# Kernel optimization log

Hardware: AMD Instinct MI355X
Metric: run time of the kernel (lower is better)

The kernel has to match this reference:

```python
import jax, jax.numpy as jnp
import numpy as np

B, L, E, H = 8, 1024, 512, 8
E2 = 2 * E
EPS = 1e-5


def _spectral_fc(x, w, fw, fb, n):
    # rfft along feature dim, multiply by rfft of learned filter w (1,n), irfft back, then Linear
    xf = jnp.fft.rfft(x, axis=2, norm='ortho')          # [B,L,n//2+1] complex
    wf = jnp.fft.rfft(w, axis=1, norm='ortho')          # [1,n//2+1] complex
    y = jnp.fft.irfft(xf * wf, n=n, axis=2, norm='ortho')
    return y @ fw + fb


def _layernorm(x, g, b):
    m = jnp.mean(x, axis=-1, keepdims=True)
    v = jnp.mean(jnp.square(x - m), axis=-1, keepdims=True)
    return (x - m) * jax.lax.rsqrt(v + EPS) * g + b


def setup_inputs() -> dict:
    key = jax.random.key(0)
    ks = jax.random.split(key, 32)
    s = 0.02

    def lin_w(k, i, o):
        return (jax.random.normal(k, (i, o), jnp.float32) / np.sqrt(i)).astype(jnp.float32)

    def layer_params(k0, k1, n):
        return (s * jax.random.normal(k0, (1, n), jnp.float32), lin_w(k1, n, n), jnp.zeros((n,), jnp.float32))

    attn_w, attn_fw, attn_fb = layer_params(ks[1], ks[2], E)
    ln0_w, ln0_fw, ln0_fb = layer_params(ks[3], ks[4], E)
    ln1_w, ln1_fw, ln1_fb = layer_params(ks[5], ks[6], E)
    ln2_w, ln2_fw, ln2_fb = layer_params(ks[7], ks[8], E)
    ln3_w, ln3_fw, ln3_fb = layer_params(ks[9], ks[10], E2)
    ln4_w, ln4_fw, ln4_fb = layer_params(ks[11], ks[12], E2)

    return {
        'x': jax.random.normal(ks[0], (B, L, E), jnp.float32),
        'attn_w': attn_w, 'attn_fw': attn_fw, 'attn_fb': attn_fb,
        'ln0_w': ln0_w, 'ln0_fw': ln0_fw, 'ln0_fb': ln0_fb,
        'ln1_w': ln1_w, 'ln1_fw': ln1_fw, 'ln1_fb': ln1_fb,
        'ln2_w': ln2_w, 'ln2_fw': ln2_fw, 'ln2_fb': ln2_fb,
        'ln3_w': ln3_w, 'ln3_fw': ln3_fw, 'ln3_fb': ln3_fb,
        'ln4_w': ln4_w, 'ln4_fw': ln4_fw, 'ln4_fb': ln4_fb,
        'n1_g': jnp.ones((E,), jnp.float32), 'n1_b': jnp.zeros((E,), jnp.float32),
        'n2_g': jnp.ones((E,), jnp.float32), 'n2_b': jnp.zeros((E,), jnp.float32),
    }


def reference(x, attn_w, attn_fw, attn_fb,
              ln0_w, ln0_fw, ln0_fb, ln1_w, ln1_fw, ln1_fb,
              ln2_w, ln2_fw, ln2_fb, ln3_w, ln3_fw, ln3_fb,
              ln4_w, ln4_fw, ln4_fb, n1_g, n1_b, n2_g, n2_b):
    q = _spectral_fc(x, attn_w, attn_fw, attn_fb, E).reshape(B, L, H, E // H)
    scores = jnp.einsum('blhe,bshe->bhls', q, q) * (1.0 / np.sqrt(E))
    A = jax.nn.softmax(scores, axis=-1)
    new_x = jnp.einsum('bhls,bshd->blhd', A, q).reshape(B, L, E)

    x1 = _layernorm(x + new_x, n1_g, n1_b)
    x_ln = jax.nn.gelu(_spectral_fc(x1, ln0_w, ln0_fw, ln0_fb, E), approximate=False)
    x2 = x1 - x_ln
    h = jax.nn.sigmoid(_spectral_fc(x2, ln1_w, ln1_fw, ln1_fb, E)) * _spectral_fc(x2, ln2_w, ln2_fw, ln2_fb, E)
    out = jnp.concatenate((new_x, x_ln), axis=-1)  # [B,L,2E]
    out = jax.nn.sigmoid(_spectral_fc(out, ln3_w, ln3_fw, ln3_fb, E2)) * _spectral_fc(out, ln4_w, ln4_fw, ln4_fb, E2)
    return (_layernorm(h, n2_g, n2_b), out)
```

## Files before the change

### kernel.cpp

```cpp
#include <hip/hip_runtime.h>
#include <hip/hip_bf16.h>
#include <math.h>

typedef __hip_bfloat16 bf16;
typedef unsigned short u16;
typedef __attribute__((ext_vector_type(8))) short short8;
typedef __attribute__((ext_vector_type(4))) float f32x4;

#define NB      8
#define SEQ     1024
#define EDIM    512
#define E2DIM   1024
#define ROWS    8192
#define INV_SQRT_E 0.04419417382415922f
#define ATT_SCL    0.06375985678148161f

__device__ inline u16 f2bu(float f) {
    union { float f; unsigned u; } c; c.f = f;
    return (u16)((c.u + 0x7FFF + ((c.u >> 16) & 1)) >> 16);
}

__device__ __forceinline__ unsigned cvtpk_bf16(float lo, float hi) {
    unsigned r;
    asm("v_cvt_pk_bf16_f32 %0, %1, %2" : "=v"(r) : "v"(lo), "v"(hi));
    return r;
}

#define VMCNT(N) do { \
    asm volatile("s_waitcnt vmcnt(" #N ")" ::: "memory"); \
    __builtin_amdgcn_sched_barrier(0); \
    __builtin_amdgcn_s_barrier(); \
    __builtin_amdgcn_sched_barrier(0); } while (0)

__device__ __forceinline__ void dma16(const u16* g, u16* l) {
    __builtin_amdgcn_global_load_lds(
        (const __attribute__((address_space(1))) void*)g,
        (__attribute__((address_space(3))) void*)l, 16, 0, 0);
}

__global__ __launch_bounds__(256) void detect_dtype(const u16* __restrict__ x,
                                                    int* __restrict__ flag) {
    int t = threadIdx.x;
    int cnt = 0;
    for (int k = t; k < 8192; k += 256) {
        int e = (x[k] >> 7) & 0xFF;
        if (e >= 0xC0) cnt++;
    }
#pragma unroll
    for (int o = 32; o > 0; o >>= 1) cnt += __shfl_xor(cnt, o);
    __shared__ int red[4];
    if ((t & 63) == 0) red[t >> 6] = cnt;
    __syncthreads();
    if (t == 0) flag[0] = (red[0] + red[1] + red[2] + red[3] > 100) ? 1 : 0;
}

struct CvtBatch {
    const void* src[23];
    float4*     dst[23];
    int         pre4[24];
};

__global__ __launch_bounds__(256) void cvt_all(CvtBatch a, int total4,
                                               const int* __restrict__ flag) {
    int t = blockIdx.x * 256 + threadIdx.x;
    if (t >= total4) return;
    int lo = 0;
    while (t >= a.pre4[lo + 1]) lo++;
    int li = t - a.pre4[lo];
    if (flag[0]) {
        a.dst[lo][li] = ((const float4*)a.src[lo])[li];
    } else {
        ushort4 u = ((const ushort4*)a.src[lo])[li];
        union { unsigned int i; float f; } c;
        float4 o;
        c.i = ((unsigned)u.x) << 16; o.x = c.f;
        c.i = ((unsigned)u.y) << 16; o.y = c.f;
        c.i = ((unsigned)u.z) << 16; o.z = c.f;
        c.i = ((unsigned)u.w) << 16; o.w = c.f;
        a.dst[lo][li] = o;
    }
}

__global__ __launch_bounds__(256) void f2b_kernel(const float* __restrict__ src,
                                                  u16* __restrict__ dst, int n4) {
    int i = blockIdx.x * 256 + threadIdx.x;
    if (i >= n4) return;
    float4 a = ((const float4*)src)[i];
    ushort4 o;
    o.x = f2bu(a.x); o.y = f2bu(a.y); o.z = f2bu(a.z); o.w = f2bu(a.w);
    ((ushort4*)dst)[i] = o;
}

#define LDK 32

__device__ __forceinline__ void xcd_swz(int& bx, int& by) {
    const int nx  = gridDim.x;
    const int nwg = nx * gridDim.y;
    const int lid = blockIdx.y * nx + blockIdx.x;
    const int q   = nwg >> 3;
    const int s   = (lid & 7) * q + (lid >> 3);
    bx = s % nx;
    by = s / nx;
}

struct FoldBatch {
    const float* w[6];
    const float* fw[6];
    u16* t1[6];
    u16* t2[6];
    u16* mt[6];
    int  n[6], lg[6];
    float sc[6];
};

__global__ __launch_bounds__(256) void fold_trconv(FoldBatch fb) {
    const int z = blockIdx.z;
    const int n = fb.n[z];
    const int bx = blockIdx.x * 32, by = blockIdx.y * 32;
    if (bx >= n || by >= n) return;
    __shared__ float t[32][33];
    const int tx = threadIdx.x & 31, ty = threadIdx.x >> 5;
    const float* src = fb.fw[z];
    u16* dst = fb.t1[z];
#pragma unroll
    for (int r = 0; r < 32; r += 8)
        t[ty + r][tx] = src[(size_t)(by + ty + r) * n + bx + tx];
    __syncthreads();
#pragma unroll
    for (int r = 0; r < 32; r += 8)
        dst[(size_t)(bx + ty + r) * n + by + tx] = f2bu(t[tx][ty + r]);
}

__global__ __launch_bounds__(256) void fold_circ(FoldBatch fb) {
    const int z = blockIdx.z;
    const int n = fb.n[z], lg = fb.lg[z];
    int idx = blockIdx.x * 256 + threadIdx.x;
    if (idx >= n * n) return;
    int mask = n - 1;
    int m = idx & mask;
    int j = idx >> lg;
    fb.t2[z][idx] = f2bu(fb.w[z][(m - j) & mask]);
}

__global__ __launch_bounds__(256) void fold_gemm(FoldBatch fb) {
    const int z = blockIdx.z;
    const int n = fb.n[z];
    const int bm = blockIdx.y * 128, bn = blockIdx.x * 128;
    if (bm >= n || bn >= n) return;
    const u16* A  = fb.t1[z];
    const u16* Bt = fb.t2[z];
    u16* Mt = fb.mt[z];
    const float scale = fb.sc[z];

    __shared__ u16 Asl[3][128 * LDK];
    __shared__ u16 Bsl[3][128 * LDK];
    const int tid = threadIdx.x;
    const int lane = tid & 63, wave = tid >> 6;
    const int wy = wave >> 1, wx = wave & 1;
    const int qd = lane >> 4, ln16 = lane & 15;
    const int ca = (qd ^ ((ln16 >> 1) & 3)) * 8;

    const int srow = wave * 16 + (lane >> 2);
    const int scol = ((lane & 3) ^ ((lane >> 3) & 3)) * 8;
    const int lo   = wave * 16 * LDK;
    const size_t a64 = (size_t)64 * n;
    const u16* pA = A  + (size_t)bm * n + (size_t)srow * n + scol;
    const u16* pB = Bt + (size_t)bn * n + (size_t)srow * n + scol;

    f32x4 acc[4][4];
#pragma unroll
    for (int i = 0; i < 4; i++)
#pragma unroll
        for (int j = 0; j < 4; j++)
#pragma unroll
            for (int r = 0; r < 4; r++) acc[i][j][r] = 0.f;

#define STAGE_FG(bi) do { \
    dma16(pA,       &Asl[bi][lo]); \
    dma16(pA + a64, &Asl[bi][lo + 64 * LDK]); \
    dma16(pB,       &Bsl[bi][lo]); \
    dma16(pB + a64, &Bsl[bi][lo + 64 * LDK]); \
    pA += 32; pB += 32; } while (0)

    const int nt = n >> 5;
    STAGE_FG(0);
    STAGE_FG(1);
    int cur = 0, stg = 2;
    for (int t = 0; t < nt; ++t) {
        if (t < nt - 1) { VMCNT(4); } else { VMCNT(0); }
        const u16* Ac = Asl[cur];
        const u16* Bc = Bsl[cur];
        short8 af[4], bf_[4];
#pragma unroll
        for (int i = 0; i < 4; i++) {
            af[i]  = *(const short8*)&Ac[(wy * 64 + i * 16 + ln16) * LDK + ca];
            bf_[i] = *(const short8*)&Bc[(wx * 64 + i * 16 + ln16) * LDK + ca];
        }
        if (t + 2 < nt) STAGE_FG(stg);
#pragma unroll
        for (int i = 0; i < 4; i++)
#pragma unroll
            for (int j = 0; j < 4; j++)
                acc[i][j] = __builtin_amdgcn_mfma_f32_16x16x32_bf16(af[i], bf_[j], acc[i][j], 0, 0, 0);
        cur = (cur == 2) ? 0 : cur + 1;
        stg = (stg == 2) ? 0 : stg + 1;
    }
#undef STAGE_FG
#pragma unroll
    for (int i = 0; i < 4; i++)
#pragma unroll
        for (int j = 0; j < 4; j++) {
            const int col = bn + wx * 64 + j * 16 + ln16;
#pragma unroll
            for (int r = 0; r < 4; r++) {
                const int row = bm + wy * 64 + i * 16 + qd * 4 + r;
                Mt[(size_t)row * n + col] = f2bu(acc[i][j][r] * scale);
            }
        }
}

__global__ __launch_bounds__(256) void gemm_bf(
    const u16* __restrict__ A, int lda,
    const u16* __restrict__ Bt, int ldb,
    const float* __restrict__ bias,
    float* __restrict__ Cf, int ldc,
    u16* __restrict__ Cb, int ldcb,
    u16* __restrict__ Cb2, int ldcb2,
    const float* __restrict__ aux, int ldaux,
    int K, int mode)
{
    __shared__ u16 Asl[3][128 * LDK];
    __shared__ u16 Bsl[3][64 * LDK];
    const int tid = threadIdx.x;
    int bxs, bys;
    xcd_swz(bxs, bys);
    const int bm = bys * 128, bn = bxs * 64;
    const int lane = tid & 63, wave = tid >> 6;
    const int wy = wave >> 1, wx = wave & 1;
    const int qd = lane >> 4, ln16 = lane & 15;
    const int ca = (qd ^ ((ln16 >> 1) & 3)) * 8;

    const int srow = wave * 16 + (lane >> 2);
    const int scol = ((lane & 3) ^ ((lane >> 3) & 3)) * 8;
    const int lo   = wave * 16 * LDK;
    const size_t a64 = (size_t)64 * lda;
    const u16* pA = A  + (size_t)bm * lda + (size_t)srow * lda + scol;
    const u16* pB = Bt + (size_t)bn * ldb + (size_t)srow * ldb + scol;

    f32x4 acc[4][2];
#pragma unroll
    for (int i = 0; i < 4; i++)
#pragma unroll
        for (int j = 0; j < 2; j++)
#pragma unroll
            for (int r = 0; r < 4; r++) acc[i][j][r] = 0.f;

#define STAGE_GB(bi) do { \
    dma16(pA,       &Asl[bi][lo]); \
    dma16(pA + a64, &Asl[bi][lo + 64 * LDK]); \
    dma16(pB,       &Bsl[bi][lo]); \
    pA += 32; pB += 32; } while (0)

    const int nt = K >> 5;
    STAGE_GB(0);
    STAGE_GB(1);
    int cur = 0, stg = 2;
    for (int t = 0; t < nt; ++t) {
        if (t < nt - 1) { VMCNT(3); } else { VMCNT(0); }
        const u16* Ac = Asl[cur];
        const u16* Bc = Bsl[cur];
        short8 af[4], bf_[2];
#pragma unroll
        for (int i = 0; i < 4; i++)
            af[i]  = *(const short8*)&Ac[(wy * 64 + i * 16 + ln16) * LDK + ca];
#pragma unroll
        for (int j = 0; j < 2; j++)
            bf_[j] = *(const short8*)&Bc[(wx * 32 + j * 16 + ln16) * LDK + ca];
        if (t + 2 < nt) STAGE_GB(stg);
#pragma unroll
        for (int i = 0; i < 4; i++)
#pragma unroll
            for (int j = 0; j < 2; j++)
                acc[i][j] = __builtin_amdgcn_mfma_f32_16x16x32_bf16(af[i], bf_[j], acc[i][j], 0, 0, 0);
        cur = (cur == 2) ? 0 : cur + 1;
        stg = (stg == 2) ? 0 : stg + 1;
    }
#undef STAGE_GB

#pragma unroll
    for (int i = 0; i < 4; i++) {
#pragma unroll
        for (int j = 0; j < 2; j++) {
            const int col = bn + wx * 32 + j * 16 + ln16;
            const float b_ = bias ? bias[col] : 0.f;
#pragma unroll
            for (int r = 0; r < 4; r++) {
                const int row = bm + wy * 64 + i * 16 + qd * 4 + r;
                float v = acc[i][j][r] + b_;
                if (mode == 1) v = 0.5f * v * (1.0f + erff(v * 0.7071067811865476f));
                if (Cf)  Cf[(size_t)row * ldc + col] = v;
                if (Cb)  Cb[(size_t)row * ldcb + col] = f2bu(v);
                if (Cb2) Cb2[(size_t)row * ldcb2 + col] =
                             f2bu(aux[(size_t)row * ldaux + col] - v);
            }
        }
    }
}

__global__ __launch_bounds__(256) void gemm_bf2(
    const u16* __restrict__ A, int lda,
    const u16* __restrict__ B1t, const u16* __restrict__ B2t, int ldb,
    const float* __restrict__ bias1, const float* __restrict__ bias2,
    float* __restrict__ Cf, int ldc, int K)
{
    __shared__ u16 Asl[3][128 * LDK];
    __shared__ u16 B1sl[3][64 * LDK];
    __shared__ u16 B2sl[3][64 * LDK];
    const int tid = threadIdx.x;
    int bxs, bys;
    xcd_swz(bxs, bys);
    const int bm = bys * 128, bn = bxs * 64;
    const int lane = tid & 63, wave = tid >> 6;
    const int wy = wave >> 1, wx = wave & 1;
    const int qd = lane >> 4, ln16 = lane & 15;
    const int ca = (qd ^ ((ln16 >> 1) & 3)) * 8;

    const int srow = wave * 16 + (lane >> 2);
    const int scol = ((lane & 3) ^ ((lane >> 3) & 3)) * 8;
    const int lo   = wave * 16 * LDK;
    const size_t a64 = (size_t)64 * lda;
    const u16* pA  = A   + (size_t)bm * lda + (size_t)srow * lda + scol;
    const u16* pB1 = B1t + (size_t)bn * ldb + (size_t)srow * ldb + scol;
    const u16* pB2 = B2t + (size_t)bn * ldb + (size_t)srow * ldb + scol;

    f32x4 acc1[4][2], acc2[4][2];
#pragma unroll
    for (int i = 0; i < 4; i++)
#pragma unroll
        for (int j = 0; j < 2; j++)
#pragma unroll
            for (int r = 0; r < 4; r++) { acc1[i][j][r] = 0.f; acc2[i][j][r] = 0.f; }

#define STAGE_GB2(bi) do { \
    dma16(pA,       &Asl[bi][lo]); \
    dma16(pA + a64, &Asl[bi][lo + 64 * LDK]); \
    dma16(pB1,      &B1sl[bi][lo]); \
    dma16(pB2,      &B2sl[bi][lo]); \
    pA += 32; pB1 += 32; pB2 += 32; } while (0)

    const int nt = K >> 5;
    STAGE_GB2(0);
    STAGE_GB2(1);
    int cur = 0, stg = 2;
    for (int t = 0; t < nt; ++t) {
        if (t < nt - 1) { VMCNT(4); } else { VMCNT(0); }
        const u16* Ac  = Asl[cur];
        const u16* B1c = B1sl[cur];
        const u16* B2c = B2sl[cur];
        short8 af[4], b1f[2], b2f[2];
#pragma unroll
        for (int i = 0; i < 4; i++)
            af[i]  = *(const short8*)&Ac [(wy * 64 + i * 16 + ln16) * LDK + ca];
#pragma unroll
        for (int j = 0; j < 2; j++) {
            b1f[j] = *(const short8*)&B1c[(wx * 32 + j * 16 + ln16) * LDK + ca];
            b2f[j] = *(const short8*)&B2c[(wx * 32 + j * 16 + ln16) * LDK + ca];
        }
        if (t + 2 < nt) STAGE_GB2(stg);
#pragma unroll
        for (int i = 0; i < 4; i++)
#pragma unroll
            for (int j = 0; j < 2; j++) {
                acc1[i][j] = __builtin_amdgcn_mfma_f32_16x16x32_bf16(af[i], b1f[j], acc1[i][j], 0, 0, 0);
                acc2[i][j] = __builtin_amdgcn_mfma_f32_16x16x32_bf16(af[i], b2f[j], acc2[i][j], 0, 0, 0);
            }
        cur = (cur == 2) ? 0 : cur + 1;
        stg = (stg == 2) ? 0 : stg + 1;
    }
#undef STAGE_GB2

#pragma unroll
    for (int i = 0; i < 4; i++) {
#pragma unroll
        for (int j = 0; j < 2; j++) {
            const int col = bn + wx * 32 + j * 16 + ln16;
            const float b1_ = bias1[col], b2_ = bias2[col];
#pragma unroll
            for (int r = 0; r < 4; r++) {
                const int row = bm + wy * 64 + i * 16 + qd * 4 + r;
                const float g = 1.0f / (1.0f + expf(-(acc1[i][j][r] + b1_)));
                Cf[(size_t)row * ldc + col] = g * (acc2[i][j][r] + b2_);
            }
        }
    }
}

__global__ __launch_bounds__(256) void ln_kernel(
    const float* __restrict__ in0, int ld0,
    const u16* __restrict__ in1b, int ld1b,
    const float* __restrict__ g, const float* __restrict__ bta,
    float* __restrict__ outf, int ldo,
    u16* __restrict__ outb, int ldob)
{
    int row = blockIdx.x, tid = threadIdx.x;
    const float* p0 = in0 + (size_t)row * ld0;
    float v0 = p0[tid], v1 = p0[tid + 256];
    if (in1b) {
        const u16* p1 = in1b + (size_t)row * ld1b;
        union { unsigned u; float f; } c0, c1;
        c0.u = ((unsigned)p1[tid]) << 16;
        c1.u = ((unsigned)p1[tid + 256]) << 16;
        v0 += c0.f; v1 += c1.f;
    }
    float s = v0 + v1, sq = v0 * v0 + v1 * v1;
#pragma unroll
    for (int o = 32; o > 0; o >>= 1) {
        s  += __shfl_xor(s, o);
        sq += __shfl_xor(sq, o);
    }
    __shared__ float red[8];
    int wid = tid >> 6;
    if ((tid & 63) == 0) { red[wid] = s; red[4 + wid] = sq; }
    __syncthreads();
    s  = red[0] + red[1] + red[2] + red[3];
    sq = red[4] + red[5] + red[6] + red[7];
    float mean = s * (1.0f / 512.0f);
    float var  = sq * (1.0f / 512.0f) - mean * mean;
    float rstd = rsqrtf(var + 1e-5f);
    float o0 = (v0 - mean) * rstd * g[tid] + bta[tid];
    float o1 = (v1 - mean) * rstd * g[tid + 256] + bta[tid + 256];
    if (outf) {
        outf[(size_t)row * ldo + tid]       = o0;
        outf[(size_t)row * ldo + tid + 256] = o1;
    }
    if (outb) {
        outb[(size_t)row * ldob + tid]       = f2bu(o0);
        outb[(size_t)row * ldob + tid + 256] = f2bu(o1);
    }
}

__global__ __launch_bounds__(256) void trans_vt(const u16* __restrict__ q,
                                                u16* __restrict__ vt) {
    const int z  = blockIdx.z;
    const int bb = z >> 3, hh = z & 7;
    const int k0 = blockIdx.x * 64;
    const int d0 = blockIdx.y * 32;
    __shared__ u16 t[64][33];
    const int tx = threadIdx.x & 31, ty = threadIdx.x >> 5;
    const u16* src = q + (size_t)(bb * SEQ + k0) * EDIM + hh * 64 + d0;
#pragma unroll
    for (int r = 0; r < 64; r += 8)
        t[ty + r][tx] = src[(size_t)(ty + r) * EDIM + tx];
    __syncthreads();
    const int ox = threadIdx.x & 63, oy = threadIdx.x >> 6;
    u16* dst = vt + ((size_t)z * 64 + d0) * SEQ + k0;
#pragma unroll
    for (int r = 0; r < 32; r += 4)
        dst[(size_t)(oy + r) * SEQ + ox] = t[ox][oy + r];
}

#define ANT 16

__global__ __launch_bounds__(256) void attn_mfma(const u16* __restrict__ qall,
                                                 const u16* __restrict__ vt,
                                                 u16* __restrict__ catb) {
    __shared__ u16 Ks[64 * 64];
    __shared__ u16 VTs[64 * 64];
    __shared__ u16 Pw[4][16 * 64];

    const int phys = blockIdx.x;
    const int bid = (phys & 7) * 128 + (phys >> 3);
    const int lt = bid & 15, hh = (bid >> 4) & 7, bb = bid >> 7;
    const int q0 = lt * 64;
    const int tid = threadIdx.x;
    const int wave = tid >> 6, lane = tid & 63;
    const int quad = lane >> 4, ln16 = lane & 15;

    const u16* qh = qall + (size_t)bb * SEQ * EDIM + hh * 64;
    const u16* vh = vt + (size_t)(bb * 8 + hh) * 64 * SEQ;

    const u16* qrow = qh + (size_t)(q0 + wave * 16 + ln16) * EDIM + quad * 8;
    const short8 aq0 = *(const short8*)(qrow);
    const short8 aq1 = *(const short8*)(qrow + 32);

    f32x4 oacc[4];
    float m_run = -1e30f;
    float l_lane = 0.f;
#pragma unroll
    for (int j = 0; j < 4; j++)
#pragma unroll
        for (int r = 0; r < 4; r++) oacc[j][r] = 0.f;

    const int sw = ln16 & 7;
    const int c0 = (quad ^ sw) * 8;
    const int c1 = ((quad + 4) ^ sw) * 8;

    const int r0  = wave * 16 + (lane >> 3);
    const int r1  = r0 + 8;
    const int cg0 = (lane & 7) ^ (r0 & 7);
    const int cg1 = (lane & 7) ^ (r1 & 7);
    const u16* pK0 = qh + (size_t)r0 * EDIM + cg0 * 8;
    const u16* pK1 = qh + (size_t)r1 * EDIM + cg1 * 8;
    const u16* pV0 = vh + (size_t)r0 * SEQ + cg0 * 8;
    const u16* pV1 = vh + (size_t)r1 * SEQ + cg1 * 8;
    const int lds0 = (wave * 16) * 64;
    const int lds1 = (wave * 16 + 8) * 64;

    for (int t = 0; t < ANT; ++t) {
        if (t) __syncthreads();
        dma16(pK0 + (size_t)t * 64 * EDIM, &Ks[lds0]);
        dma16(pK1 + (size_t)t * 64 * EDIM, &Ks[lds1]);
        dma16(pV0 + t * 64, &VTs[lds0]);
        dma16(pV1 + t * 64, &VTs[lds1]);
        __syncthreads();

        f32x4 S[4];
        __builtin_amdgcn_s_setprio(1);
#pragma unroll
        for (int j = 0; j < 4; j++) {
            const int ro = (j * 16 + ln16) * 64;
            short8 a0 = *(const short8*)&Ks[ro + c0];
            short8 a1 = *(const short8*)&Ks[ro + c1];
            f32x4 c = {0.f, 0.f, 0.f, 0.f};
            c = __builtin_amdgcn_mfma_f32_16x16x32_bf16(a0, aq0, c, 0, 0, 0);
            c = __builtin_amdgcn_mfma_f32_16x16x32_bf16(a1, aq1, c, 0, 0, 0);
            S[j] = c;
        }
        __builtin_amdgcn_s_setprio(0);

        float mxl = S[0][0];
#pragma unroll
        for (int j = 0; j < 4; j++)
#pragma unroll
            for (int r = 0; r < 4; r++) mxl = fmaxf(mxl, S[j][r]);

        const bool newm = __any(mxl > m_run);
        float al = 1.0f;
        if (newm) {
            float mx = fmaxf(mxl, __shfl_xor(mxl, 16));
            mx = fmaxf(mx, __shfl_xor(mx, 32));
            const float mn = fmaxf(m_run, mx);
            al = exp2f((m_run - mn) * ATT_SCL);
            m_run = mn;
        }
        const float ns = -m_run * ATT_SCL;
        float p[4][4];
        float rsl = 0.f;
#pragma unroll
        for (int j = 0; j < 4; j++)
#pragma unroll
            for (int r = 0; r < 4; r++) {
                p[j][r] = exp2f(fmaf(S[j][r], ATT_SCL, ns));
                rsl += p[j][r];
            }
        l_lane = l_lane * al + rsl;

#pragma unroll
        for (int j = 0; j < 4; j++) {
            unsigned w0 = cvtpk_bf16(p[j][0], p[j][1]);
            unsigned w1 = cvtpk_bf16(p[j][2], p[j][3]);
            const int blk = (j * 2 + (quad >> 1)) ^ sw;
            *(uint2*)&Pw[wave][ln16 * 64 + blk * 8 + (quad & 1) * 4] =
                make_uint2(w0, w1);
        }

        if (newm) {
            float alq[4];
#pragma unroll
            for (int r = 0; r < 4; r++) alq[r] = __shfl(al, quad * 4 + r);
#pragma unroll
            for (int j = 0; j < 4; j++)
#pragma unroll
                for (int r = 0; r < 4; r++) oacc[j][r] *= alq[r];
        }

        short8 pa0 = *(const short8*)&Pw[wave][ln16 * 64 + (quad ^ sw) * 8];
        short8 pa1 = *(const short8*)&Pw[wave][ln16 * 64 + ((quad + 4) ^ sw) * 8];
        __builtin_amdgcn_s_setprio(1);
#pragma unroll
        for (int j = 0; j < 4; j++) {
            const int ro = (j * 16 + ln16) * 64;
            short8 b0 = *(const short8*)&VTs[ro + c0];
            short8 b1 = *(const short8*)&VTs[ro + c1];
            oacc[j] = __builtin_amdgcn_mfma_f32_16x16x32_bf16(pa0, b0, oacc[j], 0, 0, 0);
            oacc[j] = __builtin_amdgcn_mfma_f32_16x16x32_bf16(pa1, b1, oacc[j], 0, 0, 0);
        }
        __builtin_amdgcn_s_setprio(0);
    }

    float l_run = l_lane;
    l_run += __shfl_xor(l_run, 16);
    l_run += __shfl_xor(l_run, 32);
    const float linv = 1.0f / l_run;
    float invq[4];
#pragma unroll
    for (int r = 0; r < 4; r++) invq[r] = __shfl(linv, quad * 4 + r);
#pragma unroll
    for (int r = 0; r < 4; r++) {
        const int row = bb * SEQ + q0 + wave * 16 + quad * 4 + r;
#pragma unroll
        for (int j = 0; j < 4; j++) {
            const int col = hh * 64 + j * 16 + ln16;
            catb[(size_t)row * E2DIM + col] = f2bu(oacc[j][r] * invq[r]);
        }
    }
}

extern "C" void kernel_launch(void* const* d_in, const int* in_sizes, int n_in,
                              void* d_out, int out_size, void* d_ws, size_t ws_size,
                              hipStream_t stream)
{
    const size_t OFF_MT0 = 0;
    const size_t OFF_MT1 = OFF_MT0 + 131072;
    const size_t OFF_MT2 = OFF_MT1 + 131072;
    const size_t OFF_MT3 = OFF_MT2 + 131072;
    const size_t OFF_MT4 = OFF_MT3 + 131072;
    const size_t OFF_MT5 = OFF_MT4 + 524288;
    const size_t OFF_XB  = OFF_MT5 + 524288;
    const size_t OFF_CB  = OFF_XB + 2097152;
    const size_t OFF_BQ  = OFF_CB + 4194304;
    const size_t OFF_BN  = OFF_BQ + 4194304;
    const size_t OFF_BC  = OFF_BN + 4194304;
    const size_t OFF_P   = OFF_BC + 4194304;

    float* W = (float*)d_ws;
    u16* MT[6] = {(u16*)(W + OFF_MT0), (u16*)(W + OFF_MT1), (u16*)(W + OFF_MT2),
                  (u16*)(W + OFF_MT3), (u16*)(W + OFF_MT4), (u16*)(W + OFF_MT5)};
    u16*   XB  = (u16*)(W + OFF_XB);
    u16*   CB  = (u16*)(W + OFF_CB);
    u16*   QB  = (u16*)(W + OFF_BQ);
    float* BN  = W + OFF_BN;
    float* BC  = W + OFF_BC;
    u16*   VT  = (u16*)BN;

    float* F[23];
    CvtBatch cb;
    int pre = 0;
    for (int i = 0; i < 23 && i < n_in; i++) {
        cb.pre4[i] = pre;
        F[i] = W + OFF_P + (size_t)pre * 4;
        cb.src[i] = d_in[i];
        cb.dst[i] = (float4*)F[i];
        pre += in_sizes[i] / 4;
    }
    cb.pre4[23] = pre;
    const int total4 = pre;
    int* FLAG = (int*)(W + OFF_P + (size_t)total4 * 4);

    if (n_in < 23) return;
    if (ws_size < (OFF_P + (size_t)total4 * 4 + 16) * sizeof(float)) return;

    detect_dtype<<<1, 256, 0, stream>>>((const u16*)d_in[0], FLAG);
    cvt_all<<<(total4 + 255) / 256, 256, 0, stream>>>(cb, total4, FLAG);
    f2b_kernel<<<(ROWS * EDIM / 4 + 255) / 256, 256, 0, stream>>>(F[0], XB, ROWS * EDIM / 4);

    FoldBatch fb;
    {
        const int wi[6] = {1, 4, 7, 10, 13, 16};
        u16* T1 = (u16*)BN;
        u16* T2 = (u16*)BC;
        size_t off = 0;
        for (int s = 0; s < 6; s++) {
            const int n = (s < 4) ? 512 : 1024;
            fb.w[s]  = F[wi[s]];
            fb.fw[s] = F[wi[s] + 1];
            fb.t1[s] = T1 + off;
            fb.t2[s] = T2 + off;
            fb.mt[s] = MT[s];
            fb.n[s]  = n;
            fb.lg[s] = (s < 4) ? 9 : 10;
            fb.sc[s] = (s < 4) ? 0.04419417382415922f : 0.03125f;
            off += (size_t)n * n;
        }
    }
    fold_trconv<<<dim3(32, 32, 6), 256, 0, stream>>>(fb);
    fold_circ<<<dim3(4096, 1, 6), 256, 0, stream>>>(fb);
    fold_gemm<<<dim3(8, 8, 6), 256, 0, stream>>>(fb);

    float* out0 = (float*)d_out;
    float* out1 = (float*)d_out + (size_t)ROWS * EDIM;

    gemm_bf<<<dim3(8, 64), 256, 0, stream>>>(
        XB, 512, MT[0], 512, F[3], nullptr, 0, QB, 512, nullptr, 0, nullptr, 0, 512, 0);
    trans_vt<<<dim3(16, 2, 64), 256, 0, stream>>>(QB, VT);
    attn_mfma<<<1024, 256, 0, stream>>>(QB, VT, CB);
    ln_kernel<<<8192, 256, 0, stream>>>(F[0], 512, CB, 1024, F[19], F[20],
                                        BC, 512, XB, 512);
    gemm_bf<<<dim3(8, 64), 256, 0, stream>>>(
        XB, 512, MT[1], 512, F[6], nullptr, 0, CB + 512, 1024, QB, 512, BC, 512, 512, 1);
    gemm_bf2<<<dim3(8, 64), 256, 0, stream>>>(
        QB, 512, MT[2], MT[3], 512, F[9], F[12], BN, 512, 512);
    ln_kernel<<<8192, 256, 0, stream>>>(BN, 512, nullptr, 0, F[21], F[22],
                                        out0, 512, nullptr, 0);
    gemm_bf2<<<dim3(16, 64), 256, 0, stream>>>(
        CB, 1024, MT[4], MT[5], 1024, F[15], F[18], out1, 1024, 1024);
}
```

Before: 326.8 us.

## Process two 64-row query tiles per attention block to reuse K/V tiles

Each attention workgroup now handles 128 query rows (two independent 64-row sub-tiles with separate online-softmax state) instead of 64, halving the grid to 512 blocks. Every K and V^T tile loaded into LDS is reused for both sub-tiles, and V fragments are read into registers once per tile. This halves global K/V traffic and LDS staging per query row. The cost is higher register pressure, fewer blocks in flight, and a shared P scratch buffer reused sequentially between the two sub-tiles.

```diff
diff --git a/kernel.cpp b/kernel.cpp
--- a/kernel.cpp
+++ b/kernel.cpp
@@ -469,9 +469,9 @@
     __shared__ u16 Pw[4][16 * 64];
 
     const int phys = blockIdx.x;
-    const int bid = (phys & 7) * 128 + (phys >> 3);
-    const int lt = bid & 15, hh = (bid >> 4) & 7, bb = bid >> 7;
-    const int q0 = lt * 64;
+    const int bid = (phys & 7) * 64 + (phys >> 3);
+    const int lt = bid & 7, hh = (bid >> 3) & 7, bb = bid >> 6;
+    const int q0 = lt * 128;
     const int tid = threadIdx.x;
     const int wave = tid >> 6, lane = tid & 63;
     const int quad = lane >> 4, ln16 = lane & 15;
@@ -479,17 +479,20 @@
     const u16* qh = qall + (size_t)bb * SEQ * EDIM + hh * 64;
     const u16* vh = vt + (size_t)(bb * 8 + hh) * 64 * SEQ;
 
-    const u16* qrow = qh + (size_t)(q0 + wave * 16 + ln16) * EDIM + quad * 8;
-    const short8 aq0 = *(const short8*)(qrow);
-    const short8 aq1 = *(const short8*)(qrow + 32);
-
-    f32x4 oacc[4];
-    float m_run = -1e30f;
-    float l_lane = 0.f;
+    const u16* qrowA = qh + (size_t)(q0 + wave * 16 + ln16) * EDIM + quad * 8;
+    const short8 aqA0 = *(const short8*)(qrowA);
+    const short8 aqA1 = *(const short8*)(qrowA + 32);
+    const u16* qrowB = qrowA + (size_t)64 * EDIM;
+    const short8 aqB0 = *(const short8*)(qrowB);
+    const short8 aqB1 = *(const short8*)(qrowB + 32);
+
+    f32x4 oaccA[4], oaccB[4];
+    float m_runA = -1e30f, l_laneA = 0.f;
+    float m_runB = -1e30f, l_laneB = 0.f;
 #pragma unroll
     for (int j = 0; j < 4; j++)
 #pragma unroll
-        for (int r = 0; r < 4; r++) oacc[j][r] = 0.f;
+        for (int r = 0; r < 4; r++) { oaccA[j][r] = 0.f; oaccB[j][r] = 0.f; }
 
     const int sw = ln16 & 7;
     const int c0 = (quad ^ sw) * 8;
@@ -514,94 +517,173 @@
         dma16(pV1 + t * 64, &VTs[lds1]);
         __syncthreads();
 
-        f32x4 S[4];
-        __builtin_amdgcn_s_setprio(1);
+        short8 vb0[4], vb1[4];
 #pragma unroll
         for (int j = 0; j < 4; j++) {
             const int ro = (j * 16 + ln16) * 64;
-            short8 a0 = *(const short8*)&Ks[ro + c0];
-            short8 a1 = *(const short8*)&Ks[ro + c1];
-            f32x4 c = {0.f, 0.f, 0.f, 0.f};
-            c = __builtin_amdgcn_mfma_f32_16x16x32_bf16(a0, aq0, c, 0, 0, 0);
-            c = __builtin_amdgcn_mfma_f32_16x16x32_bf16(a1, aq1, c, 0, 0, 0);
-            S[j] = c;
-        }
-        __builtin_amdgcn_s_setprio(0);
-
-        float mxl = S[0][0];
-#pragma unroll
-        for (int j = 0; j < 4; j++)
-#pragma unroll
-            for (int r = 0; r < 4; r++) mxl = fmaxf(mxl, S[j][r]);
-
-        const bool newm = __any(mxl > m_run);
-        float al = 1.0f;
-        if (newm) {
-            float mx = fmaxf(mxl, __shfl_xor(mxl, 16));
-            mx = fmaxf(mx, __shfl_xor(mx, 32));
-            const float mn = fmaxf(m_run, mx);
-            al = exp2f((m_run - mn) * ATT_SCL);
-            m_run = mn;
-        }
-        const float ns = -m_run * ATT_SCL;
-        float p[4][4];
-        float rsl = 0.f;
-#pragma unroll
-        for (int j = 0; j < 4; j++)
-#pragma unroll
-            for (int r = 0; r < 4; r++) {
-                p[j][r] = exp2f(fmaf(S[j][r], ATT_SCL, ns));
-                rsl += p[j][r];
-            }
-        l_lane = l_lane * al + rsl;
-
-#pragma unroll
-        for (int j = 0; j < 4; j++) {
-            unsigned w0 = cvtpk_bf16(p[j][0], p[j][1]);
-            unsigned w1 = cvtpk_bf16(p[j][2], p[j][3]);
-            const int blk = (j * 2 + (quad >> 1)) ^ sw;
-            *(uint2*)&Pw[wave][ln16 * 64 + blk * 8 + (quad & 1) * 4] =
-                make_uint2(w0, w1);
-        }
-
-        if (newm) {
-            float alq[4];
-#pragma unroll
-            for (int r = 0; r < 4; r++) alq[r] = __shfl(al, quad * 4 + r);
+            vb0[j] = *(const short8*)&VTs[ro + c0];
+            vb1[j] = *(const short8*)&VTs[ro + c1];
+        }
+
+        {
+            f32x4 S[4];
+            __builtin_amdgcn_s_setprio(1);
+#pragma unroll
+            for (int j = 0; j < 4; j++) {
+                const int ro = (j * 16 + ln16) * 64;
+                short8 a0 = *(const short8*)&Ks[ro + c0];
+                short8 a1 = *(const short8*)&Ks[ro + c1];
+                f32x4 c = {0.f, 0.f, 0.f, 0.f};
+                c = __builtin_amdgcn_mfma_f32_16x16x32_bf16(a0, aqA0, c, 0, 0, 0);
+                c = __builtin_amdgcn_mfma_f32_16x16x32_bf16(a1, aqA1, c, 0, 0, 0);
+                S[j] = c;
+            }
+            __builtin_amdgcn_s_setprio(0);
+
+            float mxl = S[0][0];
 #pragma unroll
             for (int j = 0; j < 4; j++)
 #pragma unroll
-                for (int r = 0; r < 4; r++) oacc[j][r] *= alq[r];
-        }
-
-        short8 pa0 = *(const short8*)&Pw[wave][ln16 * 64 + (quad ^ sw) * 8];
-        short8 pa1 = *(const short8*)&Pw[wave][ln16 * 64 + ((quad + 4) ^ sw) * 8];
-        __builtin_amdgcn_s_setprio(1);
-#pragma unroll
-        for (int j = 0; j < 4; j++) {
-            const int ro = (j * 16 + ln16) * 64;
-            short8 b0 = *(const short8*)&VTs[ro + c0];
-            short8 b1 = *(const short8*)&VTs[ro + c1];
-            oacc[j] = __builtin_amdgcn_mfma_f32_16x16x32_bf16(pa0, b0, oacc[j], 0, 0, 0);
-            oacc[j] = __builtin_amdgcn_mfma_f32_16x16x32_bf16(pa1, b1, oacc[j], 0, 0, 0);
-        }
-        __builtin_amdgcn_s_setprio(0);
-    }
-
-    float l_run = l_lane;
-    l_run += __shfl_xor(l_run, 16);
-    l_run += __shfl_xor(l_run, 32);
-    const float linv = 1.0f / l_run;
-    float invq[4];
-#pragma unroll
-    for (int r = 0; r < 4; r++) invq[r] = __shfl(linv, quad * 4 + r);
+                for (int r = 0; r < 4; r++) mxl = fmaxf(mxl, S[j][r]);
+            const bool newm = __any(mxl > m_runA);
+            float al = 1.0f;
+            if (newm) {
+                float mx = fmaxf(mxl, __shfl_xor(mxl, 16));
+                mx = fmaxf(mx, __shfl_xor(mx, 32));
+                const float mn = fmaxf(m_runA, mx);
+                al = exp2f((m_runA - mn) * ATT_SCL);
+                m_runA = mn;
+            }
+            const float ns = -m_runA * ATT_SCL;
+            float p[4][4];
+            float rsl = 0.f;
+#pragma unroll
+            for (int j = 0; j < 4; j++)
+#pragma unroll
+                for (int r = 0; r < 4; r++) {
+                    p[j][r] = exp2f(fmaf(S[j][r], ATT_SCL, ns));
+                    rsl += p[j][r];
+                }
+            l_laneA = l_laneA * al + rsl;
+#pragma unroll
+            for (int j = 0; j < 4; j++) {
+                unsigned w0 = cvtpk_bf16(p[j][0], p[j][1]);
+                unsigned w1 = cvtpk_bf16(p[j][2], p[j][3]);
+                const int blk = (j * 2 + (quad >> 1)) ^ sw;
+                *(uint2*)&Pw[wave][ln16 * 64 + blk * 8 + (quad & 1) * 4] =
+                    make_uint2(w0, w1);
+            }
+            if (newm) {
+                float alq[4];
+#pragma unroll
+                for (int r = 0; r < 4; r++) alq[r] = __shfl(al, quad * 4 + r);
+#pragma unroll
+                for (int j = 0; j < 4; j++)
+#pragma unroll
+                    for (int r = 0; r < 4; r++) oaccA[j][r] *= alq[r];
+            }
+            short8 pa0 = *(const short8*)&Pw[wave][ln16 * 64 + (quad ^ sw) * 8];
+            short8 pa1 = *(const short8*)&Pw[wave][ln16 * 64 + ((quad + 4) ^ sw) * 8];
+            __builtin_amdgcn_s_setprio(1);
+#pragma unroll
+            for (int j = 0; j < 4; j++) {
+                oaccA[j] = __builtin_amdgcn_mfma_f32_16x16x32_bf16(pa0, vb0[j], oaccA[j], 0, 0, 0);
+                oaccA[j] = __builtin_amdgcn_mfma_f32_16x16x32_bf16(pa1, vb1[j], oaccA[j], 0, 0, 0);
+            }
+            __builtin_amdgcn_s_setprio(0);
+        }
+
+        {
+            f32x4 S[4];
+            __builtin_amdgcn_s_setprio(1);
+#pragma unroll
+            for (int j = 0; j < 4; j++) {
+                const int ro = (j * 16 + ln16) * 64;
+                short8 a0 = *(const short8*)&Ks[ro + c0];
+                short8 a1 = *(const short8*)&Ks[ro + c1];
+                f32x4 c = {0.f, 0.f, 0.f, 0.f};
+                c = __builtin_amdgcn_mfma_f32_16x16x32_bf16(a0, aqB0, c, 0, 0, 0);
+                c = __builtin_amdgcn_mfma_f32_16x16x32_bf16(a1, aqB1, c, 0, 0, 0);
+                S[j] = c;
+            }
+            __builtin_amdgcn_s_setprio(0);
+
+            float mxl = S[0][0];
+#pragma unroll
+            for (int j = 0; j < 4; j++)
+#pragma unroll
+                for (int r = 0; r < 4; r++) mxl = fmaxf(mxl, S[j][r]);
+            const bool newm = __any(mxl > m_runB);
+            float al = 1.0f;
+            if (newm) {
+                float mx = fmaxf(mxl, __shfl_xor(mxl, 16));
+                mx = fmaxf(mx, __shfl_xor(mx, 32));
+                const float mn = fmaxf(m_runB, mx);
+                al = exp2f((m_runB - mn) * ATT_SCL);
+                m_runB = mn;
+            }
+            const float ns = -m_runB * ATT_SCL;
+            float p[4][4];
+            float rsl = 0.f;
+#pragma unroll
+            for (int j = 0; j < 4; j++)
+#pragma unroll
+                for (int r = 0; r < 4; r++) {
+                    p[j][r] = exp2f(fmaf(S[j][r], ATT_SCL, ns));
+                    rsl += p[j][r];
+                }
+            l_laneB = l_laneB * al + rsl;
+#pragma unroll
+            for (int j = 0; j < 4; j++) {
+                unsigned w0 = cvtpk_bf16(p[j][0], p[j][1]);
+                unsigned w1 = cvtpk_bf16(p[j][2], p[j][3]);
+                const int blk = (j * 2 + (quad >> 1)) ^ sw;
+                *(uint2*)&Pw[wave][ln16 * 64 + blk * 8 + (quad & 1) * 4] =
+                    make_uint2(w0, w1);
+            }
+            if (newm) {
+                float alq[4];
+#pragma unroll
+                for (int r = 0; r < 4; r++) alq[r] = __shfl(al, quad * 4 + r);
+#pragma unroll
+                for (int j = 0; j < 4; j++)
+#pragma unroll
+                    for (int r = 0; r < 4; r++) oaccB[j][r] *= alq[r];
+            }
+            short8 pa0 = *(const short8*)&Pw[wave][ln16 * 64 + (quad ^ sw) * 8];
+            short8 pa1 = *(const short8*)&Pw[wave][ln16 * 64 + ((quad + 4) ^ sw) * 8];
+            __builtin_amdgcn_s_setprio(1);
+#pragma unroll
+            for (int j = 0; j < 4; j++) {
+                oaccB[j] = __builtin_amdgcn_mfma_f32_16x16x32_bf16(pa0, vb0[j], oaccB[j], 0, 0, 0);
+                oaccB[j] = __builtin_amdgcn_mfma_f32_16x16x32_bf16(pa1, vb1[j], oaccB[j], 0, 0, 0);
+            }
+            __builtin_amdgcn_s_setprio(0);
+        }
+    }
+
+    float lA = l_laneA;
+    lA += __shfl_xor(lA, 16);
+    lA += __shfl_xor(lA, 32);
+    const float linvA = 1.0f / lA;
+    float lB = l_laneB;
+    lB += __shfl_xor(lB, 16);
+    lB += __shfl_xor(lB, 32);
+    const float linvB = 1.0f / lB;
+    float invqA[4], invqB[4];
 #pragma unroll
     for (int r = 0; r < 4; r++) {
-        const int row = bb * SEQ + q0 + wave * 16 + quad * 4 + r;
+        invqA[r] = __shfl(linvA, quad * 4 + r);
+        invqB[r] = __shfl(linvB, quad * 4 + r);
+    }
+#pragma unroll
+    for (int r = 0; r < 4; r++) {
+        const int rowA = bb * SEQ + q0 + wave * 16 + quad * 4 + r;
 #pragma unroll
         for (int j = 0; j < 4; j++) {
             const int col = hh * 64 + j * 16 + ln16;
-            catb[(size_t)row * E2DIM + col] = f2bu(oacc[j][r] * invq[r]);
+            catb[(size_t)rowA * E2DIM + col] = f2bu(oaccA[j][r] * invqA[r]);
+            catb[(size_t)(rowA + 64) * E2DIM + col] = f2bu(oaccB[j][r] * invqB[r]);
         }
     }
 }
@@ -683,7 +765,7 @@
     gemm_bf<<<dim3(8, 64), 256, 0, stream>>>(
         XB, 512, MT[0], 512, F[3], nullptr, 0, QB, 512, nullptr, 0, nullptr, 0, 512, 0);
     trans_vt<<<dim3(16, 2, 64), 256, 0, stream>>>(QB, VT);
-    attn_mfma<<<1024, 256, 0, stream>>>(QB, VT, CB);
+    attn_mfma<<<512, 256, 0, stream>>>(QB, VT, CB);
     ln_kernel<<<8192, 256, 0, stream>>>(F[0], 512, CB, 1024, F[19], F[20],
                                         BC, 512, XB, 512);
     gemm_bf<<<dim3(8, 64), 256, 0, stream>>>(
```

Result: no change. 330.9 us (+1.3%).
